# Optimization experiments

Measured on AMD Instinct MI355X. Metric: run time of the kernel, lower is better.

## Reference

```python
import jax, jax.numpy as jnp
import numpy as np

N = 100000   # nodes
E = 1600000  # edges (avg degree 16)
DIN, DH, DOUT = 128, 64, 40


def setup_inputs() -> dict:
    key = jax.random.key(0)
    ks = jax.random.split(key, 6)
    x = jax.random.normal(ks[0], (N, DIN), dtype=jnp.float32)
    edge_index = jax.random.randint(ks[1], (2, E), 0, N, dtype=jnp.int32)
    s1 = float(1.0 / np.sqrt(DIN))
    s2 = float(1.0 / np.sqrt(DH))
    W1 = jax.random.uniform(ks[2], (DIN, DH), jnp.float32, -s1, s1)
    b1 = jax.random.uniform(ks[3], (DH,), jnp.float32, -s1, s1)
    W2 = jax.random.uniform(ks[4], (DH, DOUT), jnp.float32, -s2, s2)
    b2 = jax.random.uniform(ks[5], (DOUT,), jnp.float32, -s2, s2)
    return {"x": x, "W1": W1, "b1": b1, "W2": W2, "b2": b2, "edge_index": edge_index}


def _gcn_conv(x, W, b, src, dst):
    """PyG GCNConv: add self-loops, symmetric degree normalization, scatter-add."""
    n = x.shape[0]
    h = x @ W  # [N, F_out] — transform before propagation (PyG order)
    ones = jnp.ones(src.shape[0], dtype=h.dtype)
    deg = jax.ops.segment_sum(ones, dst, num_segments=n) + 1.0  # +1 for self-loop
    dinv = jax.lax.rsqrt(deg)  # deg >= 1, no zero guard needed
    norm = dinv[src] * dinv[dst]  # [E]
    agg = jax.ops.segment_sum(h[src] * norm[:, None], dst, num_segments=n)
    agg = agg + h * (dinv * dinv)[:, None]  # self-loop messages
    return agg + b


def reference(x, W1, b1, W2, b2, edge_index):
    src, dst = edge_index[0], edge_index[1]
    h = jax.nn.relu(_gcn_conv(x, W1, b1, src, dst))
    out = _gcn_conv(h, W2, b2, src, dst)
    return jax.nn.log_softmax(out, axis=1)
```

## Files before the change

### kernel.cpp

```cpp
#include <hip/hip_runtime.h>
#include <math.h>

#define N_NODES 100000
#define N_EDGES 1600000
#define DIN 128
#define DH 64
#define DOUT 40

#define NB 256
#define BN 391
#define CAP 8192
#define BIN_BLOCKS 1024
#define EPB 1563

typedef unsigned short u16;
typedef unsigned int u32;

__device__ inline float bf2f(u16 u) {
    return __uint_as_float(((u32)u) << 16);
}
__device__ inline u16 f2bf(float f) {
    u32 u = __float_as_uint(f);
    u32 r = (u + 0x7FFFu + ((u >> 16) & 1u)) >> 16;
    return (u16)r;
}


__global__ __launch_bounds__(256) void k_bin(const int* __restrict__ src,
                                             const int* __restrict__ dst,
                                             int* __restrict__ gcur,
                                             u32* __restrict__ staged) {
    __shared__ int hist[NB];
    __shared__ int base[NB];
    __shared__ int cur[NB];
    int t = threadIdx.x;
    for (int i = t; i < NB; i += 256) { hist[i] = 0; cur[i] = 0; }
    __syncthreads();
    int e0 = blockIdx.x * EPB;
    int e1 = e0 + EPB; if (e1 > N_EDGES) e1 = N_EDGES;
    for (int e = e0 + t; e < e1; e += 256)
        atomicAdd(&hist[dst[e] / BN], 1);
    __syncthreads();
    for (int i = t; i < NB; i += 256) {
        int h = hist[i];
        base[i] = h ? atomicAdd(&gcur[i], h) : 0;
    }
    __syncthreads();
    for (int e = e0 + t; e < e1; e += 256) {
        int d = dst[e], s = src[e];
        int b = d / BN;
        int dl = d - b * BN;
        int r = base[b] + atomicAdd(&cur[b], 1);
        if (r < CAP) staged[(size_t)b * CAP + r] = (u32)s | ((u32)dl << 17);
    }
}


__global__ __launch_bounds__(256) void k_csr(const int* __restrict__ gcur,
                                             const u32* __restrict__ staged,
                                             int* __restrict__ csr,
                                             int* __restrict__ rs,
                                             int* __restrict__ deg,
                                             float* __restrict__ dinv) {
    __shared__ u32 sedge[CAP];
    __shared__ int lcsr[CAP];
    __shared__ int hist[BN];
    __shared__ int lrs[BN];
    __shared__ int cur[BN];
    __shared__ int sbuf[256];
    int b = blockIdx.x, t = threadIdx.x;

    int part = 0;
    for (int i = t; i < b; i += 256) {
        int c = gcur[i]; if (c > CAP) c = CAP;
        part += c;
    }
    sbuf[t] = part;
    __syncthreads();
    for (int off = 128; off; off >>= 1) {
        if (t < off) sbuf[t] += sbuf[t + off];
        __syncthreads();
    }
    int base_ = sbuf[0];
    __syncthreads();

    int cnt = gcur[b]; if (cnt > CAP) cnt = CAP;
    for (int i = t; i < BN; i += 256) hist[i] = 0;
    for (int i = t; i < cnt; i += 256) sedge[i] = staged[(size_t)b * CAP + i];
    __syncthreads();
    for (int i = t; i < cnt; i += 256) atomicAdd(&hist[sedge[i] >> 17], 1);
    __syncthreads();

    int v0 = (2 * t < BN) ? hist[2 * t] : 0;
    int v1 = (2 * t + 1 < BN) ? hist[2 * t + 1] : 0;
    int s = v0 + v1;
    sbuf[t] = s;
    __syncthreads();
    for (int off = 1; off < 256; off <<= 1) {
        int add = (t >= off) ? sbuf[t - off] : 0;
        __syncthreads();
        sbuf[t] += add;
        __syncthreads();
    }
    int excl = sbuf[t] - s;
    if (2 * t < BN)     { lrs[2 * t] = excl;      cur[2 * t] = excl; }
    if (2 * t + 1 < BN) { lrs[2 * t + 1] = excl + v0; cur[2 * t + 1] = excl + v0; }
    __syncthreads();

    for (int i = t; i < cnt; i += 256) {
        u32 p = sedge[i];
        int pos = atomicAdd(&cur[p >> 17], 1);
        lcsr[pos] = (int)(p & 0x1FFFF);
    }
    __syncthreads();

    for (int i = t; i < cnt; i += 256) csr[base_ + i] = lcsr[i];
    int n0 = b * BN;
    for (int i = t; i < BN; i += 256) {
        int n = n0 + i;
        if (n < N_NODES) {
            int dg = hist[i];
            rs[n] = base_ + lrs[i];
            deg[n] = dg;
            dinv[n] = rsqrtf((float)dg + 1.0f);
        }
    }
}


__global__ __launch_bounds__(256) void k_gemm1(const float* __restrict__ x,
                                               const float* __restrict__ W1,
                                               const float* __restrict__ dinv,
                                               u16* __restrict__ h1s) {
    __shared__ float xs[64 * 132];
    __shared__ float wsh[DIN * DH];
    int t = threadIdx.x;
    int row0 = blockIdx.x * 64;

    for (int it = 0; it < 8; ++it) {
        int idx = (it * 256 + t) * 4;
        int r = idx >> 7, c = idx & 127;
        float4 v = make_float4(0.f, 0.f, 0.f, 0.f);
        if (row0 + r < N_NODES) v = *(const float4*)&x[(size_t)(row0 + r) * DIN + c];
        *(float4*)&xs[r * 132 + c] = v;
    }
    for (int it = 0; it < 8; ++it) {
        int idx = (it * 256 + t) * 4;
        *(float4*)&wsh[idx] = *(const float4*)&W1[idx];
    }
    __syncthreads();

    int tr = t & 15;
    int tc = t >> 4;
    float acc[4][4] = {};
    for (int k = 0; k < DIN; ++k) {
        float4 wv = *(const float4*)&wsh[k * DH + tr * 4];
#pragma unroll
        for (int i = 0; i < 4; ++i) {
            float xv = xs[(tc * 4 + i) * 132 + k];
            acc[i][0] += xv * wv.x;
            acc[i][1] += xv * wv.y;
            acc[i][2] += xv * wv.z;
            acc[i][3] += xv * wv.w;
        }
    }
#pragma unroll
    for (int i = 0; i < 4; ++i) {
        int row = row0 + tc * 4 + i;
        if (row < N_NODES) {
            float dv = dinv[row];
            ushort4 o;
            o.x = f2bf(acc[i][0] * dv);
            o.y = f2bf(acc[i][1] * dv);
            o.z = f2bf(acc[i][2] * dv);
            o.w = f2bf(acc[i][3] * dv);
            *(ushort4*)&h1s[(size_t)row * DH + tr * 4] = o;
        }
    }
}


__global__ __launch_bounds__(256) void k_agg1(const u16* __restrict__ h1s,
                                              const int* __restrict__ rs,
                                              const int* __restrict__ deg,
                                              const int* __restrict__ csr,
                                              const float* __restrict__ dinv,
                                              const float* __restrict__ b1,
                                              float* __restrict__ h1) {
    int node = blockIdx.x * 4 + (threadIdx.x >> 6);
    int lane = threadIdx.x & 63;
    if (node >= N_NODES) return;
    int s0 = rs[node];
    int d = deg[node];
    float a0 = bf2f(h1s[(size_t)node * DH + lane]);
    float a1 = 0.f, a2 = 0.f, a3 = 0.f, a4 = 0.f, a5 = 0.f, a6 = 0.f, a7 = 0.f;
    for (int base = 0; base < d; base += 64) {
        int nn = d - base; if (nn > 64) nn = 64;
        int myidx = (lane < nn) ? csr[s0 + base + lane] : 0;
        int j = 0;
        for (; j + 8 <= nn; j += 8) {
            int i0 = __shfl(myidx, j + 0, 64); int i1 = __shfl(myidx, j + 1, 64);
            int i2 = __shfl(myidx, j + 2, 64); int i3 = __shfl(myidx, j + 3, 64);
            int i4 = __shfl(myidx, j + 4, 64); int i5 = __shfl(myidx, j + 5, 64);
            int i6 = __shfl(myidx, j + 6, 64); int i7 = __shfl(myidx, j + 7, 64);
            a0 += bf2f(h1s[(size_t)i0 * DH + lane]);
            a1 += bf2f(h1s[(size_t)i1 * DH + lane]);
            a2 += bf2f(h1s[(size_t)i2 * DH + lane]);
            a3 += bf2f(h1s[(size_t)i3 * DH + lane]);
            a4 += bf2f(h1s[(size_t)i4 * DH + lane]);
            a5 += bf2f(h1s[(size_t)i5 * DH + lane]);
            a6 += bf2f(h1s[(size_t)i6 * DH + lane]);
            a7 += bf2f(h1s[(size_t)i7 * DH + lane]);
        }
        for (; j < nn; ++j) {
            int s = __shfl(myidx, j, 64);
            a0 += bf2f(h1s[(size_t)s * DH + lane]);
        }
    }
    float acc = ((a0 + a1) + (a2 + a3)) + ((a4 + a5) + (a6 + a7));
    float v = acc * dinv[node] + b1[lane];
    h1[(size_t)node * DH + lane] = fmaxf(v, 0.f);
}


__global__ __launch_bounds__(256) void k_gemm2(const float* __restrict__ h1,
                                               const float* __restrict__ W2,
                                               const float* __restrict__ dinv,
                                               u16* __restrict__ h2s) {
    __shared__ float xs[64 * 68];
    __shared__ float wsh[DH * DOUT];
    int t = threadIdx.x;
    int row0 = blockIdx.x * 64;

    for (int it = 0; it < 4; ++it) {
        int idx = (it * 256 + t) * 4;
        int r = idx >> 6, c = idx & 63;
        float4 v = make_float4(0.f, 0.f, 0.f, 0.f);
        if (row0 + r < N_NODES) v = *(const float4*)&h1[(size_t)(row0 + r) * DH + c];
        *(float4*)&xs[r * 68 + c] = v;
    }
    for (int idx = t * 4; idx < DH * DOUT; idx += 1024) {
        *(float4*)&wsh[idx] = *(const float4*)&W2[idx];
    }
    __syncthreads();

    int fg = t & 7;
    int rg = t >> 3;
    float acc[2][5] = {};
    for (int k = 0; k < DH; ++k) {
        float x0 = xs[(rg * 2 + 0) * 68 + k];
        float x1 = xs[(rg * 2 + 1) * 68 + k];
#pragma unroll
        for (int j = 0; j < 5; ++j) {
            float w = wsh[k * DOUT + fg * 5 + j];
            acc[0][j] += x0 * w;
            acc[1][j] += x1 * w;
        }
    }
#pragma unroll
    for (int i = 0; i < 2; ++i) {
        int row = row0 + rg * 2 + i;
        if (row < N_NODES) {
            float dv = dinv[row];
#pragma unroll
            for (int j = 0; j < 5; ++j)
                h2s[(size_t)row * 64 + fg * 5 + j] = f2bf(acc[i][j] * dv);
        }
    }
}


__global__ __launch_bounds__(256) void k_agg2(const u16* __restrict__ h2s,
                                              const int* __restrict__ rs,
                                              const int* __restrict__ deg,
                                              const int* __restrict__ csr,
                                              const float* __restrict__ dinv,
                                              const float* __restrict__ b2,
                                              float* __restrict__ out) {
    int node = blockIdx.x * 4 + (threadIdx.x >> 6);
    int lane = threadIdx.x & 63;
    if (node >= N_NODES) return;
    int s0 = rs[node];
    int d = deg[node];
    bool act = lane < DOUT;
    float a0 = act ? bf2f(h2s[(size_t)node * 64 + lane]) : 0.f;
    float a1 = 0.f, a2 = 0.f, a3 = 0.f, a4 = 0.f, a5 = 0.f, a6 = 0.f, a7 = 0.f;
    for (int base = 0; base < d; base += 64) {
        int nn = d - base; if (nn > 64) nn = 64;
        int myidx = (lane < nn) ? csr[s0 + base + lane] : 0;
        int j = 0;
        for (; j + 8 <= nn; j += 8) {
            int i0 = __shfl(myidx, j + 0, 64); int i1 = __shfl(myidx, j + 1, 64);
            int i2 = __shfl(myidx, j + 2, 64); int i3 = __shfl(myidx, j + 3, 64);
            int i4 = __shfl(myidx, j + 4, 64); int i5 = __shfl(myidx, j + 5, 64);
            int i6 = __shfl(myidx, j + 6, 64); int i7 = __shfl(myidx, j + 7, 64);
            if (act) {
                a0 += bf2f(h2s[(size_t)i0 * 64 + lane]);
                a1 += bf2f(h2s[(size_t)i1 * 64 + lane]);
                a2 += bf2f(h2s[(size_t)i2 * 64 + lane]);
                a3 += bf2f(h2s[(size_t)i3 * 64 + lane]);
                a4 += bf2f(h2s[(size_t)i4 * 64 + lane]);
                a5 += bf2f(h2s[(size_t)i5 * 64 + lane]);
                a6 += bf2f(h2s[(size_t)i6 * 64 + lane]);
                a7 += bf2f(h2s[(size_t)i7 * 64 + lane]);
            }
        }
        for (; j < nn; ++j) {
            int s = __shfl(myidx, j, 64);
            if (act) a0 += bf2f(h2s[(size_t)s * 64 + lane]);
        }
    }
    float acc = ((a0 + a1) + (a2 + a3)) + ((a4 + a5) + (a6 + a7));
    float v = act ? acc * dinv[node] + b2[lane] : -INFINITY;
    float m = v;
    for (int off = 32; off; off >>= 1) m = fmaxf(m, __shfl_xor(m, off, 64));
    float ex = act ? expf(v - m) : 0.f;
    float sum = ex;
    for (int off = 32; off; off >>= 1) sum += __shfl_xor(sum, off, 64);
    float lse = m + logf(sum);
    if (act) out[(size_t)node * DOUT + lane] = v - lse;
}


extern "C" void kernel_launch(void* const* d_in, const int* in_sizes, int n_in,
                              void* d_out, int out_size, void* d_ws, size_t ws_size,
                              hipStream_t stream) {
    const float* x  = (const float*)d_in[0];
    const float* W1 = (const float*)d_in[1];
    const float* b1 = (const float*)d_in[2];
    const float* W2 = (const float*)d_in[3];
    const float* b2 = (const float*)d_in[4];
    const int* eidx = (const int*)d_in[5];
    const int* srcp = eidx;
    const int* dstp = eidx + N_EDGES;
    float* out = (float*)d_out;

    char* w = (char*)d_ws;
    int* gcur    = (int*)w;   w += sizeof(int) * NB;
    float* dinv  = (float*)w; w += sizeof(float) * N_NODES;
    int* rs      = (int*)w;   w += sizeof(int) * N_NODES;
    int* deg     = (int*)w;   w += sizeof(int) * N_NODES;
    u32* staged  = (u32*)w;   w += sizeof(u32) * (size_t)NB * CAP;
    int* csr     = (int*)w;   w += sizeof(int) * N_EDGES;
    u16* h1s     = (u16*)w;   w += sizeof(u16) * (size_t)N_NODES * DH;
    float* h1    = (float*)w; w += sizeof(float) * (size_t)N_NODES * DH;
    u16* h2s     = h1s;

    hipMemsetAsync(gcur, 0, sizeof(int) * NB, stream);
    k_bin<<<BIN_BLOCKS, 256, 0, stream>>>(srcp, dstp, gcur, staged);
    k_csr<<<NB, 256, 0, stream>>>(gcur, staged, csr, rs, deg, dinv);
    k_gemm1<<<(N_NODES + 63) / 64, 256, 0, stream>>>(x, W1, dinv, h1s);
    k_agg1<<<(N_NODES + 3) / 4, 256, 0, stream>>>(h1s, rs, deg, csr, dinv, b1, h1);
    k_gemm2<<<(N_NODES + 63) / 64, 256, 0, stream>>>(h1, W2, dinv, h2s);
    k_agg2<<<(N_NODES + 3) / 4, 256, 0, stream>>>(h2s, rs, deg, csr, dinv, b2, out);
}
```

Before: 245.5 us.

## Vectorize aggregation gathers with 8-byte loads across four edge slots per wave

Both aggregation kernels now split each 64-lane wave into four groups of 16 lanes. Each group gathers a different neighbor row with 8-byte (4 x bf16) loads, and the partial sums are combined by cross-lane shuffle reductions. Per-node row start, degree and dinv are packed into one int4 metadata array, so a single load replaces three. The log-softmax works on four values per lane and stores float4 output. The edge-binning kernel also uses half as many blocks, each handling twice as many edges. The aim is fewer, wider memory transactions and fewer shuffle instructions per edge, at the cost of an extra reduction step and idle lanes in agg2.

```diff
diff --git a/kernel.cpp b/kernel.cpp
--- a/kernel.cpp
+++ b/kernel.cpp
@@ -10,8 +10,8 @@
 #define NB 256
 #define BN 391
 #define CAP 8192
-#define BIN_BLOCKS 1024
-#define EPB 1563
+#define BIN_BLOCKS 512
+#define EPB 3125
 
 typedef unsigned short u16;
 typedef unsigned int u32;
@@ -23,6 +23,12 @@
     u32 u = __float_as_uint(f);
     u32 r = (u + 0x7FFFu + ((u >> 16) & 1u)) >> 16;
     return (u16)r;
+}
+__device__ inline void acc4(uint2 v, float& a0, float& a1, float& a2, float& a3) {
+    a0 += __uint_as_float(v.x << 16);
+    a1 += __uint_as_float(v.x & 0xffff0000u);
+    a2 += __uint_as_float(v.y << 16);
+    a3 += __uint_as_float(v.y & 0xffff0000u);
 }
 
 
@@ -59,8 +65,7 @@
 __global__ __launch_bounds__(256) void k_csr(const int* __restrict__ gcur,
                                              const u32* __restrict__ staged,
                                              int* __restrict__ csr,
-                                             int* __restrict__ rs,
-                                             int* __restrict__ deg,
+                                             int4* __restrict__ meta,
                                              float* __restrict__ dinv) {
     __shared__ u32 sedge[CAP];
     __shared__ int lcsr[CAP];
@@ -120,9 +125,9 @@
         int n = n0 + i;
         if (n < N_NODES) {
             int dg = hist[i];
-            rs[n] = base_ + lrs[i];
-            deg[n] = dg;
-            dinv[n] = rsqrtf((float)dg + 1.0f);
+            float dv = rsqrtf((float)dg + 1.0f);
+            meta[n] = make_int4(base_ + lrs[i], dg, __float_as_int(dv), 0);
+            dinv[n] = dv;
         }
     }
 }
@@ -181,45 +186,57 @@
 
 
 __global__ __launch_bounds__(256) void k_agg1(const u16* __restrict__ h1s,
-                                              const int* __restrict__ rs,
-                                              const int* __restrict__ deg,
+                                              const int4* __restrict__ meta,
                                               const int* __restrict__ csr,
-                                              const float* __restrict__ dinv,
                                               const float* __restrict__ b1,
                                               float* __restrict__ h1) {
     int node = blockIdx.x * 4 + (threadIdx.x >> 6);
+    if (node >= N_NODES) return;
+    node = __builtin_amdgcn_readfirstlane(node);
     int lane = threadIdx.x & 63;
-    if (node >= N_NODES) return;
-    int s0 = rs[node];
-    int d = deg[node];
-    float a0 = bf2f(h1s[(size_t)node * DH + lane]);
-    float a1 = 0.f, a2 = 0.f, a3 = 0.f, a4 = 0.f, a5 = 0.f, a6 = 0.f, a7 = 0.f;
+    int es = lane >> 4, fp = lane & 15;
+    int4 me = meta[node];
+    int s0 = me.x, d = me.y;
+    float dv = __int_as_float(me.z);
+    const uint2* rows = (const uint2*)h1s;
+    float a0 = 0.f, a1 = 0.f, a2 = 0.f, a3 = 0.f;
+    if (es == 0) acc4(rows[(u32)(node * 16 + fp)], a0, a1, a2, a3);
     for (int base = 0; base < d; base += 64) {
         int nn = d - base; if (nn > 64) nn = 64;
         int myidx = (lane < nn) ? csr[s0 + base + lane] : 0;
         int j = 0;
-        for (; j + 8 <= nn; j += 8) {
-            int i0 = __shfl(myidx, j + 0, 64); int i1 = __shfl(myidx, j + 1, 64);
-            int i2 = __shfl(myidx, j + 2, 64); int i3 = __shfl(myidx, j + 3, 64);
-            int i4 = __shfl(myidx, j + 4, 64); int i5 = __shfl(myidx, j + 5, 64);
-            int i6 = __shfl(myidx, j + 6, 64); int i7 = __shfl(myidx, j + 7, 64);
-            a0 += bf2f(h1s[(size_t)i0 * DH + lane]);
-            a1 += bf2f(h1s[(size_t)i1 * DH + lane]);
-            a2 += bf2f(h1s[(size_t)i2 * DH + lane]);
-            a3 += bf2f(h1s[(size_t)i3 * DH + lane]);
-            a4 += bf2f(h1s[(size_t)i4 * DH + lane]);
-            a5 += bf2f(h1s[(size_t)i5 * DH + lane]);
-            a6 += bf2f(h1s[(size_t)i6 * DH + lane]);
-            a7 += bf2f(h1s[(size_t)i7 * DH + lane]);
-        }
-        for (; j < nn; ++j) {
-            int s = __shfl(myidx, j, 64);
-            a0 += bf2f(h1s[(size_t)s * DH + lane]);
-        }
-    }
-    float acc = ((a0 + a1) + (a2 + a3)) + ((a4 + a5) + (a6 + a7));
-    float v = acc * dinv[node] + b1[lane];
-    h1[(size_t)node * DH + lane] = fmaxf(v, 0.f);
+        for (; j + 16 <= nn; j += 16) {
+            int x0 = __builtin_amdgcn_ds_bpermute((j + es) * 4, myidx);
+            int x1 = __builtin_amdgcn_ds_bpermute((j + 4 + es) * 4, myidx);
+            int x2 = __builtin_amdgcn_ds_bpermute((j + 8 + es) * 4, myidx);
+            int x3 = __builtin_amdgcn_ds_bpermute((j + 12 + es) * 4, myidx);
+            uint2 v0 = rows[(u32)(x0 * 16 + fp)];
+            uint2 v1 = rows[(u32)(x1 * 16 + fp)];
+            uint2 v2 = rows[(u32)(x2 * 16 + fp)];
+            uint2 v3 = rows[(u32)(x3 * 16 + fp)];
+            acc4(v0, a0, a1, a2, a3);
+            acc4(v1, a0, a1, a2, a3);
+            acc4(v2, a0, a1, a2, a3);
+            acc4(v3, a0, a1, a2, a3);
+        }
+        for (; j < nn; j += 4) {
+            int x = __builtin_amdgcn_ds_bpermute((j + es) * 4, myidx);
+            if (j + es < nn) acc4(rows[(u32)(x * 16 + fp)], a0, a1, a2, a3);
+        }
+    }
+    a0 += __shfl_xor(a0, 16, 64); a1 += __shfl_xor(a1, 16, 64);
+    a2 += __shfl_xor(a2, 16, 64); a3 += __shfl_xor(a3, 16, 64);
+    a0 += __shfl_xor(a0, 32, 64); a1 += __shfl_xor(a1, 32, 64);
+    a2 += __shfl_xor(a2, 32, 64); a3 += __shfl_xor(a3, 32, 64);
+    if (es == 0) {
+        float4 bv = ((const float4*)b1)[fp];
+        float4 o;
+        o.x = fmaxf(a0 * dv + bv.x, 0.f);
+        o.y = fmaxf(a1 * dv + bv.y, 0.f);
+        o.z = fmaxf(a2 * dv + bv.z, 0.f);
+        o.w = fmaxf(a3 * dv + bv.w, 0.f);
+        ((float4*)h1)[(u32)(node * 16 + fp)] = o;
+    }
 }
 
 
@@ -261,64 +278,82 @@
     for (int i = 0; i < 2; ++i) {
         int row = row0 + rg * 2 + i;
         if (row < N_NODES) {
-            float dv = dinv[row];
+            float dvv = dinv[row];
 #pragma unroll
             for (int j = 0; j < 5; ++j)
-                h2s[(size_t)row * 64 + fg * 5 + j] = f2bf(acc[i][j] * dv);
+                h2s[(size_t)row * 64 + fg * 5 + j] = f2bf(acc[i][j] * dvv);
         }
     }
 }
 
 
 __global__ __launch_bounds__(256) void k_agg2(const u16* __restrict__ h2s,
-                                              const int* __restrict__ rs,
-                                              const int* __restrict__ deg,
+                                              const int4* __restrict__ meta,
                                               const int* __restrict__ csr,
-                                              const float* __restrict__ dinv,
                                               const float* __restrict__ b2,
                                               float* __restrict__ out) {
     int node = blockIdx.x * 4 + (threadIdx.x >> 6);
+    if (node >= N_NODES) return;
+    node = __builtin_amdgcn_readfirstlane(node);
     int lane = threadIdx.x & 63;
-    if (node >= N_NODES) return;
-    int s0 = rs[node];
-    int d = deg[node];
-    bool act = lane < DOUT;
-    float a0 = act ? bf2f(h2s[(size_t)node * 64 + lane]) : 0.f;
-    float a1 = 0.f, a2 = 0.f, a3 = 0.f, a4 = 0.f, a5 = 0.f, a6 = 0.f, a7 = 0.f;
+    int es = lane >> 4, fp = lane & 15;
+    bool act = fp < 10;
+    int4 me = meta[node];
+    int s0 = me.x, d = me.y;
+    float dv = __int_as_float(me.z);
+    const uint2* rows = (const uint2*)h2s;
+    float a0 = 0.f, a1 = 0.f, a2 = 0.f, a3 = 0.f;
+    if (es == 0 && act) acc4(rows[(u32)(node * 16 + fp)], a0, a1, a2, a3);
     for (int base = 0; base < d; base += 64) {
         int nn = d - base; if (nn > 64) nn = 64;
         int myidx = (lane < nn) ? csr[s0 + base + lane] : 0;
         int j = 0;
-        for (; j + 8 <= nn; j += 8) {
-            int i0 = __shfl(myidx, j + 0, 64); int i1 = __shfl(myidx, j + 1, 64);
-            int i2 = __shfl(myidx, j + 2, 64); int i3 = __shfl(myidx, j + 3, 64);
-            int i4 = __shfl(myidx, j + 4, 64); int i5 = __shfl(myidx, j + 5, 64);
-            int i6 = __shfl(myidx, j + 6, 64); int i7 = __shfl(myidx, j + 7, 64);
+        for (; j + 16 <= nn; j += 16) {
+            int x0 = __builtin_amdgcn_ds_bpermute((j + es) * 4, myidx);
+            int x1 = __builtin_amdgcn_ds_bpermute((j + 4 + es) * 4, myidx);
+            int x2 = __builtin_amdgcn_ds_bpermute((j + 8 + es) * 4, myidx);
+            int x3 = __builtin_amdgcn_ds_bpermute((j + 12 + es) * 4, myidx);
             if (act) {
-                a0 += bf2f(h2s[(size_t)i0 * 64 + lane]);
-                a1 += bf2f(h2s[(size_t)i1 * 64 + lane]);
-                a2 += bf2f(h2s[(size_t)i2 * 64 + lane]);
-                a3 += bf2f(h2s[(size_t)i3 * 64 + lane]);
-                a4 += bf2f(h2s[(size_t)i4 * 64 + lane]);
-                a5 += bf2f(h2s[(size_t)i5 * 64 + lane]);
-                a6 += bf2f(h2s[(size_t)i6 * 64 + lane]);
-                a7 += bf2f(h2s[(size_t)i7 * 64 + lane]);
+                uint2 v0 = rows[(u32)(x0 * 16 + fp)];
+                uint2 v1 = rows[(u32)(x1 * 16 + fp)];
+                uint2 v2 = rows[(u32)(x2 * 16 + fp)];
+                uint2 v3 = rows[(u32)(x3 * 16 + fp)];
+                acc4(v0, a0, a1, a2, a3);
+                acc4(v1, a0, a1, a2, a3);
+                acc4(v2, a0, a1, a2, a3);
+                acc4(v3, a0, a1, a2, a3);
             }
         }
-        for (; j < nn; ++j) {
-            int s = __shfl(myidx, j, 64);
-            if (act) a0 += bf2f(h2s[(size_t)s * 64 + lane]);
-        }
-    }
-    float acc = ((a0 + a1) + (a2 + a3)) + ((a4 + a5) + (a6 + a7));
-    float v = act ? acc * dinv[node] + b2[lane] : -INFINITY;
-    float m = v;
-    for (int off = 32; off; off >>= 1) m = fmaxf(m, __shfl_xor(m, off, 64));
-    float ex = act ? expf(v - m) : 0.f;
-    float sum = ex;
-    for (int off = 32; off; off >>= 1) sum += __shfl_xor(sum, off, 64);
-    float lse = m + logf(sum);
-    if (act) out[(size_t)node * DOUT + lane] = v - lse;
+        for (; j < nn; j += 4) {
+            int x = __builtin_amdgcn_ds_bpermute((j + es) * 4, myidx);
+            if (act && j + es < nn) acc4(rows[(u32)(x * 16 + fp)], a0, a1, a2, a3);
+        }
+    }
+    a0 += __shfl_xor(a0, 16, 64); a1 += __shfl_xor(a1, 16, 64);
+    a2 += __shfl_xor(a2, 16, 64); a3 += __shfl_xor(a3, 16, 64);
+    a0 += __shfl_xor(a0, 32, 64); a1 += __shfl_xor(a1, 32, 64);
+    a2 += __shfl_xor(a2, 32, 64); a3 += __shfl_xor(a3, 32, 64);
+
+    float4 bv = act ? ((const float4*)b2)[fp] : make_float4(0.f, 0.f, 0.f, 0.f);
+    float v0 = act ? a0 * dv + bv.x : -INFINITY;
+    float v1 = act ? a1 * dv + bv.y : -INFINITY;
+    float v2 = act ? a2 * dv + bv.z : -INFINITY;
+    float v3 = act ? a3 * dv + bv.w : -INFINITY;
+    float m = fmaxf(fmaxf(v0, v1), fmaxf(v2, v3));
+    m = fmaxf(m, __shfl_xor(m, 1, 64));
+    m = fmaxf(m, __shfl_xor(m, 2, 64));
+    m = fmaxf(m, __shfl_xor(m, 4, 64));
+    m = fmaxf(m, __shfl_xor(m, 8, 64));
+    float ex = act ? (expf(v0 - m) + expf(v1 - m) + expf(v2 - m) + expf(v3 - m)) : 0.f;
+    ex += __shfl_xor(ex, 1, 64);
+    ex += __shfl_xor(ex, 2, 64);
+    ex += __shfl_xor(ex, 4, 64);
+    ex += __shfl_xor(ex, 8, 64);
+    float lse = m + logf(ex);
+    if (es == 0 && act) {
+        float4 o = make_float4(v0 - lse, v1 - lse, v2 - lse, v3 - lse);
+        *(float4*)&out[(u32)(node * 40 + fp * 4)] = o;
+    }
 }
 
 
@@ -337,9 +372,8 @@
 
     char* w = (char*)d_ws;
     int* gcur    = (int*)w;   w += sizeof(int) * NB;
-    float* dinv  = (float*)w; w += sizeof(float) * N_NODES;
-    int* rs      = (int*)w;   w += sizeof(int) * N_NODES;
-    int* deg     = (int*)w;   w += sizeof(int) * N_NODES;
+    float* dinv  = (float*)w; w += sizeof(float) * N_NODES + 48;
+    int4* meta   = (int4*)w;  w += sizeof(int4) * N_NODES;
     u32* staged  = (u32*)w;   w += sizeof(u32) * (size_t)NB * CAP;
     int* csr     = (int*)w;   w += sizeof(int) * N_EDGES;
     u16* h1s     = (u16*)w;   w += sizeof(u16) * (size_t)N_NODES * DH;
@@ -348,9 +382,9 @@
 
     hipMemsetAsync(gcur, 0, sizeof(int) * NB, stream);
     k_bin<<<BIN_BLOCKS, 256, 0, stream>>>(srcp, dstp, gcur, staged);
-    k_csr<<<NB, 256, 0, stream>>>(gcur, staged, csr, rs, deg, dinv);
+    k_csr<<<NB, 256, 0, stream>>>(gcur, staged, csr, meta, dinv);
     k_gemm1<<<(N_NODES + 63) / 64, 256, 0, stream>>>(x, W1, dinv, h1s);
-    k_agg1<<<(N_NODES + 3) / 4, 256, 0, stream>>>(h1s, rs, deg, csr, dinv, b1, h1);
+    k_agg1<<<(N_NODES + 3) / 4, 256, 0, stream>>>(h1s, meta, csr, b1, h1);
     k_gemm2<<<(N_NODES + 63) / 64, 256, 0, stream>>>(h1, W2, dinv, h2s);
-    k_agg2<<<(N_NODES + 3) / 4, 256, 0, stream>>>(h2s, rs, deg, csr, dinv, b2, out);
-}
+    k_agg2<<<(N_NODES + 3) / 4, 256, 0, stream>>>(h2s, meta, csr, b2, out);
+}
```

Result: faster. 222.0 us (-9.6%).
